# Kernel tuning notes

Measured on AMD Instinct MI355X. Metric: run time of the kernel, lower is better.

The kernel has to match this reference:

```python
import jax, jax.numpy as jnp
import numpy as np

N, E0 = 50000, 800000          # nodes, raw edges (self-loops appended in reference)
IN, H, C = 128, 8, 8           # in_channels, heads, out_channels per head
ED, T = 16, 96                 # edge_dim, temporal profile length
NEG_SLOPE = 0.2                # leaky relu slope
CW = 0.5                       # complementarity_weight


def setup_inputs() -> dict:
    key = jax.random.key(0)
    ks = jax.random.split(key, 12)
    def xavier(k, shape):
        fan_in, fan_out = shape[1], shape[0]
        lim = np.sqrt(6.0 / (fan_in + fan_out)).astype(np.float32)
        return jax.random.uniform(k, shape, jnp.float32, -lim, lim)
    return {
        "x": jax.random.normal(ks[0], (N, IN), jnp.float32),
        "edge_index": jax.random.randint(ks[1], (2, E0), 0, N, jnp.int64),
        "edge_attr": jax.random.normal(ks[2], (E0, ED), jnp.float32),
        "temporal_profiles": jax.random.normal(ks[3], (N, T), jnp.float32),
        "Wq": xavier(ks[4], (H * C, IN)),
        "Wk": xavier(ks[5], (H * C, IN)),
        "Wv": xavier(ks[6], (H * C, IN)),
        "We": xavier(ks[7], (H * C, ED)),
        "comp_W": xavier(ks[8], (H, 2 * IN)),
        "comp_b": jnp.zeros((H,), jnp.float32),
        "Wo": xavier(ks[9], (C, H * C)),
        "bo": jnp.zeros((C,), jnp.float32),
    }


def reference(x, edge_index, edge_attr, temporal_profiles,
              Wq, Wk, Wv, We, comp_W, comp_b, Wo, bo):
    n = x.shape[0]
    # ---- add self loops (PyG add_self_loops; edge_attr filled with 1.0) ----
    loops = jnp.arange(n, dtype=edge_index.dtype)
    ei = jnp.concatenate([edge_index, jnp.stack([loops, loops])], axis=1)
    ea = jnp.concatenate(
        [edge_attr, jnp.ones((n, edge_attr.shape[1]), edge_attr.dtype)], axis=0)
    src, dst = ei[0], ei[1]  # key/value side (j) = src, query side (i) = dst

    # ---- node projections [N, H, C] ----
    q = (x @ Wq.T).reshape(n, H, C)
    k = (x @ Wk.T).reshape(n, H, C)
    v = (x @ Wv.T).reshape(n, H, C)

    # ---- complementarity scores per edge ----
    tp = temporal_profiles
    tpn = (tp - tp.mean(axis=1, keepdims=True)) / \
          (tp.std(axis=1, ddof=1, keepdims=True) + 1e-8)  # torch std is unbiased
    correlation = (tpn[src] * tpn[dst]).mean(axis=1)       # [E]
    # Linear(2*IN -> H) on concat([x[src], x[dst]]) == split matmul per node
    a_node = x @ comp_W[:, :IN].T                          # [N, H]
    b_node = x @ comp_W[:, IN:].T                          # [N, H]
    learned = jnp.tanh(a_node[src] + b_node[dst] + comp_b).mean(axis=1)
    comp = 0.5 * correlation + 0.5 * learned               # [E]

    # ---- per-edge attention logits ----
    key_j = k[src]                                         # [E, H, C]
    alpha = (q[dst] * key_j).sum(-1) / np.sqrt(C).astype(np.float32)  # [E, H]
    edge_feat = (ea @ We.T).reshape(-1, H, C)
    alpha = alpha + (edge_feat * key_j).sum(-1)
    alpha = alpha + CW * (-comp)[:, None]
    alpha = jnp.where(alpha >= 0, alpha, NEG_SLOPE * alpha)  # leaky_relu

    # ---- segment softmax over destination nodes (PyG softmax) ----
    amax = jax.ops.segment_max(alpha, dst, num_segments=n)   # every node has a self loop
    e = jnp.exp(alpha - amax[dst])
    denom = jax.ops.segment_sum(e, dst, num_segments=n)
    att = e / (denom[dst] + 1e-16)                           # [E, H]

    # ---- weighted scatter-add aggregation ----
    msg = v[src] * att[:, :, None]                           # [E, H, C]
    out = jax.ops.segment_sum(msg, dst, num_segments=n).reshape(n, H * C)
    return out @ Wo.T + bo
```

## Files before the change

### kernel.cpp

```cpp
#include <hip/hip_runtime.h>
#include <math.h>


struct __align__(8) US4 { unsigned short x, y, z, w; };

typedef __attribute__((ext_vector_type(8))) short bf16x8;
typedef __attribute__((ext_vector_type(4))) float f32x4;

#define CH 32

__device__ __forceinline__ unsigned short f2bf(float f) {
    unsigned u = __float_as_uint(f);
    unsigned r = (u + 0x7fffu + ((u >> 16) & 1u)) >> 16;
    return (unsigned short)r;
}
__device__ __forceinline__ float bf2f(unsigned short u) {
    return __uint_as_float(((unsigned)u) << 16);
}
__device__ __forceinline__ float blo(unsigned u) { return __uint_as_float(u << 16); }
__device__ __forceinline__ float bhi(unsigned u) { return __uint_as_float(u & 0xffff0000u); }

__global__ __launch_bounds__(256) void k_xcvt(const float* __restrict__ x,
                                              unsigned short* __restrict__ xb, int total4)
{
    int i = blockIdx.x * 256 + threadIdx.x;
    if (i >= total4) return;
    float4 v = ((const float4*)x)[i];
    US4 u = { f2bf(v.x), f2bf(v.y), f2bf(v.z), f2bf(v.w) };
    ((US4*)xb)[i] = u;
}

__global__ __launch_bounds__(256) void k_bpack(
    const float* __restrict__ Wq, const float* __restrict__ Wk, const float* __restrict__ Wv,
    const float* __restrict__ compW, const float* __restrict__ We,
    unsigned short* __restrict__ Bp)
{
    int gid = blockIdx.x * 256 + threadIdx.x;
    if (gid >= 21 * 2048) return;
    int i = gid & 7, lane = (gid >> 3) & 63, s = (gid >> 9) & 3, t = gid >> 11;
    int col = t * 16 + (lane & 15);
    int k = s * 32 + ((lane >> 4) << 3) + i;
    float v;
    if (col < 64)        v = Wq[col * 128 + k];
    else if (col < 128)  v = Wk[(col - 64) * 128 + k];
    else if (col < 192)  v = Wv[(col - 128) * 128 + k];
    else if (col < 200)  v = compW[(col - 192) * 256 + k];
    else if (col < 208)  v = compW[(col - 200) * 256 + 128 + k];
    else {
        int hd = col - 208, h = hd >> 4, d = hd & 15;
        v = 0.f;
        #pragma unroll
        for (int c = 0; c < 8; c++)
            v += Wk[(h * 8 + c) * 128 + k] * We[(h * 8 + c) * 16 + d];
    }
    Bp[gid] = f2bf(v);
}

__global__ __launch_bounds__(256) void k_gemm(
    const unsigned short* __restrict__ xb, const unsigned short* __restrict__ Bp,
    const float* __restrict__ compb,
    float* __restrict__ q, unsigned short* __restrict__ kb, unsigned short* __restrict__ vb,
    float* __restrict__ an, float* __restrict__ bn, unsigned short* __restrict__ Gb, int N)
{
    const int tid = threadIdx.x, w = tid >> 6, lane = tid & 63;
    const int half = lane >> 4;
    const int c0 = lane & 15;
    int row_a = blockIdx.x * 64 + w * 16 + c0;
    int ra = min(row_a, N - 1);
    bf16x8 a0 = *(const bf16x8*)(xb + (size_t)ra * 128 +  0 + half * 8);
    bf16x8 a1 = *(const bf16x8*)(xb + (size_t)ra * 128 + 32 + half * 8);
    bf16x8 a2 = *(const bf16x8*)(xb + (size_t)ra * 128 + 64 + half * 8);
    bf16x8 a3 = *(const bf16x8*)(xb + (size_t)ra * 128 + 96 + half * 8);
    const int rbase = blockIdx.x * 64 + w * 16 + half * 4;
    const float cbv = compb[c0 & 7];

    for (int t = 0; t < 21; t++) {
        f32x4 acc = {0.f, 0.f, 0.f, 0.f};
        const bf16x8* bp = (const bf16x8*)(Bp + (size_t)((t * 4) * 64 + lane) * 8);
        acc = __builtin_amdgcn_mfma_f32_16x16x32_bf16(a0, bp[0],   acc, 0, 0, 0);
        acc = __builtin_amdgcn_mfma_f32_16x16x32_bf16(a1, bp[64],  acc, 0, 0, 0);
        acc = __builtin_amdgcn_mfma_f32_16x16x32_bf16(a2, bp[128], acc, 0, 0, 0);
        acc = __builtin_amdgcn_mfma_f32_16x16x32_bf16(a3, bp[192], acc, 0, 0, 0);
        #pragma unroll
        for (int r = 0; r < 4; r++) {
            int rr = rbase + r;
            if (rr >= N) continue;
            float vr = acc[r];
            if (t < 4)        q[(size_t)rr * 64 + t * 16 + c0] = vr * 0.35355339059327373f;
            else if (t < 8)   kb[(size_t)rr * 64 + (t - 4) * 16 + c0] = f2bf(vr);
            else if (t < 12)  vb[(size_t)rr * 64 + (t - 8) * 16 + c0] = f2bf(vr);
            else if (t == 12) {
                if (c0 < 8) an[(size_t)rr * 8 + c0] = vr;
                else        bn[(size_t)rr * 8 + (c0 - 8)] = vr + cbv;
            }
            else              Gb[(size_t)rr * 128 + (t - 13) * 16 + c0] = f2bf(vr);
        }
    }
}

__global__ __launch_bounds__(256) void k_tpn(const float* __restrict__ tp,
                                             unsigned short* __restrict__ tpnb, int N)
{
    int wave = threadIdx.x >> 6;
    int lane = threadIdx.x & 63;
    int n = blockIdx.x * 4 + wave;
    if (n >= N) return;
    const float* row = tp + (size_t)n * 96;
    float v0 = row[lane];
    float v1 = (lane < 32) ? row[64 + lane] : 0.f;
    float s = v0 + v1, ss = v0 * v0 + v1 * v1;
    #pragma unroll
    for (int m = 1; m < 64; m <<= 1) { s += __shfl_xor(s, m); ss += __shfl_xor(ss, m); }
    float mean = s * (1.f / 96.f);
    float var = (ss - 96.f * mean * mean) * (1.f / 95.f);
    var = fmaxf(var, 0.f);
    float inv = 1.f / (sqrtf(var) + 1e-8f);
    unsigned short* orow = tpnb + (size_t)n * 96;
    orow[lane] = f2bf((v0 - mean) * inv);
    if (lane < 32) orow[64 + lane] = f2bf((v1 - mean) * inv);
}

__global__ __launch_bounds__(256) void k_hist(const int* __restrict__ ei,
                                              int* __restrict__ deg,
                                              int* __restrict__ rnk, int E0, int N)
{
    int e = blockIdx.x * 256 + threadIdx.x;
    int E = E0 + N;
    if (e >= E) return;
    int dst = (e < E0) ? ei[E0 + e] : (e - E0);
    rnk[e] = atomicAdd(&deg[dst], 1);
}

__global__ __launch_bounds__(256) void k_scanA(const int* __restrict__ deg,
                                               int* __restrict__ bsum, int N)
{
    __shared__ int sm[256];
    int i = blockIdx.x * 256 + threadIdx.x;
    sm[threadIdx.x] = (i < N) ? deg[i] : 0;
    __syncthreads();
    for (int off = 128; off > 0; off >>= 1) {
        if (threadIdx.x < off) sm[threadIdx.x] += sm[threadIdx.x + off];
        __syncthreads();
    }
    if (threadIdx.x == 0) bsum[blockIdx.x] = sm[0];
}

__global__ __launch_bounds__(256) void k_scanB(int* __restrict__ bsum, int NB)
{
    __shared__ int sm[256];
    int t = threadIdx.x;
    sm[t] = (t < NB) ? bsum[t] : 0;
    __syncthreads();
    for (int off = 1; off < 256; off <<= 1) {
        int v = (t >= off) ? sm[t - off] : 0;
        __syncthreads();
        sm[t] += v;
        __syncthreads();
    }
    if (t < NB) bsum[t] = (t == 0) ? 0 : sm[t - 1];
}

__global__ __launch_bounds__(256) void k_scanC(const int* __restrict__ deg,
                                               const int* __restrict__ bsum,
                                               int* __restrict__ row, int N)
{
    __shared__ int sm[256];
    int b = blockIdx.x, t = threadIdx.x, i = b * 256 + t;
    int v = (i < N) ? deg[i] : 0;
    sm[t] = v;
    __syncthreads();
    for (int off = 1; off < 256; off <<= 1) {
        int u = (t >= off) ? sm[t - off] : 0;
        __syncthreads();
        sm[t] += u;
        __syncthreads();
    }
    int excl = bsum[b] + sm[t] - v;
    if (i < N) {
        row[i] = excl;
        if (i == N - 1) row[N] = excl + v;
    }
}

__global__ __launch_bounds__(256) void k_scatter(const int* __restrict__ ei,
                                                 const int* __restrict__ row,
                                                 const int* __restrict__ rnk,
                                                 int2* __restrict__ csrd, int E0, int N)
{
    int e = blockIdx.x * 256 + threadIdx.x;
    int E = E0 + N;
    if (e >= E) return;
    int src, dst;
    if (e < E0) { src = ei[e]; dst = ei[E0 + e]; }
    else        { src = e - E0; dst = src; }
    int pos = row[dst] + rnk[e];
    csrd[pos] = make_int2(e, src);
}

__global__ __launch_bounds__(256) void k_nodeattn(
    const int2* __restrict__ csrd, const int* __restrict__ row,
    const float* __restrict__ eattr,
    const unsigned short* __restrict__ tpnb, const float* __restrict__ q,
    const unsigned short* __restrict__ kb, const unsigned short* __restrict__ Gb,
    const float* __restrict__ an, const float* __restrict__ bn,
    const unsigned short* __restrict__ vb,
    const float* __restrict__ Wo, const float* __restrict__ bo,
    float* __restrict__ out, int E0, int N)
{
    __shared__ float alsA[4][CH * 8];
    __shared__ int srcA[4][CH];
    const int tid = threadIdx.x;
    const int wave = tid >> 6, lane = tid & 63;
    const int n = blockIdx.x * 4 + wave;
    if (n >= N) return;
    float* als = alsA[wave];
    int* srcs = srcA[wave];

    const int beg = row[n], end = row[n + 1];
    const int h = lane & 7;
    const int g = lane >> 3;

    const float4* qp = (const float4*)(q + (size_t)n * 64 + h * 8);
    const float4 qd0 = qp[0], qd1 = qp[1];
    const uint2* tdp = (const uint2*)(tpnb + (size_t)n * 96 + h * 12);
    const uint2 td0 = tdp[0], td1 = tdp[1], td2 = tdp[2];
    const float bnh = bn[(size_t)n * 8 + h];

    float m_reg = -1e30f, dsum = 0.f;
    float acc[8];
    #pragma unroll
    for (int c = 0; c < 8; c++) acc[c] = 0.f;

    for (int cbeg = beg; cbeg < end; cbeg += CH) {
        const int cnt = min(CH, end - cbeg);

        #pragma unroll
        for (int j = 0; j < 4; j++) {
            int eo = g + 8 * j;
            if (eo < cnt) {
                int2 es = csrd[cbeg + eo];
                const int e = es.x, s = es.y;

                const US4* kp = (const US4*)(kb + (size_t)s * 64 + h * 8);
                US4 k0 = kp[0], k1 = kp[1];
                float qk = qd0.x*bf2f(k0.x) + qd0.y*bf2f(k0.y) + qd0.z*bf2f(k0.z) + qd0.w*bf2f(k0.w)
                         + qd1.x*bf2f(k1.x) + qd1.y*bf2f(k1.y) + qd1.z*bf2f(k1.z) + qd1.w*bf2f(k1.w);

                const uint4* gp = (const uint4*)(Gb + (size_t)s * 128 + h * 16);
                uint4 g0 = gp[0], g1 = gp[1];
                int ec = (e < E0) ? e : 0;
                const float4* ep4 = (const float4*)(eattr + (size_t)ec * 16);
                float4 e0 = ep4[0], e1 = ep4[1], e2 = ep4[2], e3 = ep4[3];
                if (e >= E0) {
                    e0 = make_float4(1.f, 1.f, 1.f, 1.f); e1 = e0; e2 = e0; e3 = e0;
                }
                float efk = e0.x*blo(g0.x) + e0.y*bhi(g0.x) + e0.z*blo(g0.y) + e0.w*bhi(g0.y)
                          + e1.x*blo(g0.z) + e1.y*bhi(g0.z) + e1.z*blo(g0.w) + e1.w*bhi(g0.w)
                          + e2.x*blo(g1.x) + e2.y*bhi(g1.x) + e2.z*blo(g1.y) + e2.w*bhi(g1.y)
                          + e3.x*blo(g1.z) + e3.y*bhi(g1.z) + e3.z*blo(g1.w) + e3.w*bhi(g1.w);

                float tv = an[(size_t)s * 8 + h] + bnh;
                float ex = __expf(2.f * tv);
                float tn = 1.f - 2.f / (ex + 1.f);

                const uint2* tsp = (const uint2*)(tpnb + (size_t)s * 96 + h * 12);
                uint2 s0 = tsp[0], s1 = tsp[1], s2 = tsp[2];
                float pc = blo(s0.x)*blo(td0.x) + bhi(s0.x)*bhi(td0.x)
                         + blo(s0.y)*blo(td0.y) + bhi(s0.y)*bhi(td0.y)
                         + blo(s1.x)*blo(td1.x) + bhi(s1.x)*bhi(td1.x)
                         + blo(s1.y)*blo(td1.y) + bhi(s1.y)*bhi(td1.y)
                         + blo(s2.x)*blo(td2.x) + bhi(s2.x)*bhi(td2.x)
                         + blo(s2.y)*blo(td2.y) + bhi(s2.y)*bhi(td2.y);
                float cv = pc * (-0.25f / 96.f) + tn * (-0.25f / 8.f);
                cv += __shfl_xor(cv, 1); cv += __shfl_xor(cv, 2); cv += __shfl_xor(cv, 4);

                float a = qk + efk + cv;
                a = fmaxf(a, 0.2f * a);
                als[eo * 8 + h] = a;
                if (h == 0) srcs[eo] = s;
            }
        }

        float mloc = -1e30f;
        #pragma unroll
        for (int r = 0; r < 4; r++) {
            int eo = g + 8 * r;
            if (eo < cnt) mloc = fmaxf(mloc, als[eo * 8 + h]);
        }
        mloc = fmaxf(mloc, __shfl_xor(mloc, 8));
        mloc = fmaxf(mloc, __shfl_xor(mloc, 16));
        mloc = fmaxf(mloc, __shfl_xor(mloc, 32));

        float mn = fmaxf(m_reg, mloc);
        float sc = __expf(m_reg - mn);
        m_reg = mn;
        dsum *= sc;
        #pragma unroll
        for (int c = 0; c < 8; c++) acc[c] *= sc;

        for (int i = g; i < cnt; i += 8) {
            float av = als[i * 8 + h];
            int s = srcs[i];
            uint4 vu = *(const uint4*)(vb + (size_t)s * 64 + h * 8);
            float p = __expf(av - mn);
            dsum += p;
            acc[0] += p * blo(vu.x); acc[1] += p * bhi(vu.x);
            acc[2] += p * blo(vu.y); acc[3] += p * bhi(vu.y);
            acc[4] += p * blo(vu.z); acc[5] += p * bhi(vu.z);
            acc[6] += p * blo(vu.w); acc[7] += p * bhi(vu.w);
        }
    }

    dsum += __shfl_xor(dsum, 8); dsum += __shfl_xor(dsum, 16); dsum += __shfl_xor(dsum, 32);
    #pragma unroll
    for (int c = 0; c < 8; c++) {
        acc[c] += __shfl_xor(acc[c], 8);
        acc[c] += __shfl_xor(acc[c], 16);
        acc[c] += __shfl_xor(acc[c], 32);
    }
    float inv = 1.f / (dsum + 1e-16f);

    float po[8];
    #pragma unroll
    for (int cp8 = 0; cp8 < 8; cp8++) {
        const float4* wr = (const float4*)(Wo + cp8 * 64 + h * 8);
        float4 w0 = wr[0], w1 = wr[1];
        po[cp8] = inv * (acc[0]*w0.x + acc[1]*w0.y + acc[2]*w0.z + acc[3]*w0.w
                       + acc[4]*w1.x + acc[5]*w1.y + acc[6]*w1.z + acc[7]*w1.w);
    }
    #pragma unroll
    for (int cp8 = 0; cp8 < 8; cp8++) {
        po[cp8] += __shfl_xor(po[cp8], 1);
        po[cp8] += __shfl_xor(po[cp8], 2);
        po[cp8] += __shfl_xor(po[cp8], 4);
    }
    if (lane < 8) out[(size_t)n * 8 + lane] = po[lane] + bo[lane];
}

extern "C" void kernel_launch(void* const* d_in, const int* in_sizes, int n_in,
                              void* d_out, int out_size, void* d_ws, size_t ws_size,
                              hipStream_t stream)
{
    const float* x     = (const float*)d_in[0];
    const int*   ei    = (const int*)d_in[1];
    const float* eattr = (const float*)d_in[2];
    const float* tp    = (const float*)d_in[3];
    const float* Wq    = (const float*)d_in[4];
    const float* Wk    = (const float*)d_in[5];
    const float* Wv    = (const float*)d_in[6];
    const float* We    = (const float*)d_in[7];
    const float* compW = (const float*)d_in[8];
    const float* compb = (const float*)d_in[9];
    const float* Wo    = (const float*)d_in[10];
    const float* bo    = (const float*)d_in[11];
    float* out = (float*)d_out;

    const int N  = in_sizes[0] / 128;
    const int E0 = in_sizes[1] / 2;
    const int E  = E0 + N;
    const int NB = (N + 255) / 256;

    float* ws = (float*)d_ws;
    size_t off = 0;
    unsigned short* tpnb = (unsigned short*)(ws + off); off += (size_t)N * 48;
    float* q  = ws + off; off += (size_t)N * 64;
    unsigned short* kb = (unsigned short*)(ws + off); off += (size_t)N * 32;
    unsigned short* vb = (unsigned short*)(ws + off); off += (size_t)N * 32;
    unsigned short* Gb = (unsigned short*)(ws + off); off += (size_t)N * 64;
    float* an = ws + off; off += (size_t)N * 8;
    float* bn = ws + off; off += (size_t)N * 8;
    int* deg    = (int*)(ws + off); off += N;
    int* bsum   = (int*)(ws + off); off += 256;
    int* rowp   = (int*)(ws + off); off += N + 4;
    unsigned short* Bp = (unsigned short*)(ws + off); off += 21504;
    int2* csrd  = (int2*)(ws + off); off += (size_t)E * 2;
    int* rnk    = (int*)(ws + off); off += E;
    unsigned short* xb = (unsigned short*)(ws + off); off += (size_t)N * 64;

    hipMemsetAsync(deg, 0, (size_t)N * sizeof(int), stream);

    k_hist<<<(E + 255) / 256, 256, 0, stream>>>(ei, deg, rnk, E0, N);
    k_scanA<<<NB, 256, 0, stream>>>(deg, bsum, N);
    k_scanB<<<1, 256, 0, stream>>>(bsum, NB);
    k_scanC<<<NB, 256, 0, stream>>>(deg, bsum, rowp, N);
    k_scatter<<<(E + 255) / 256, 256, 0, stream>>>(ei, rowp, rnk, csrd, E0, N);

    k_xcvt<<<((size_t)N * 32 + 255) / 256, 256, 0, stream>>>(x, xb, N * 32);
    k_bpack<<<(21 * 2048 + 255) / 256, 256, 0, stream>>>(Wq, Wk, Wv, compW, We, Bp);
    k_gemm<<<(N + 63) / 64, 256, 0, stream>>>(xb, Bp, compb, q, kb, vb, an, bn, Gb, N);
    k_tpn<<<(N + 3) / 4, 256, 0, stream>>>(tp, tpnb, N);

    k_nodeattn<<<(N + 3) / 4, 256, 0, stream>>>(csrd, rowp, eattr, tpnb, q, kb, Gb,
                                                an, bn, vb, Wo, bo, out, E0, N);
}
```

Measured before the change: 228.8 us.

## Fuse x bf16 conversion into GEMM and keep attention logits in registers

```diff
diff --git a/kernel.cpp b/kernel.cpp
--- a/kernel.cpp
+++ b/kernel.cpp
@@ -19,16 +19,6 @@
 }
 __device__ __forceinline__ float blo(unsigned u) { return __uint_as_float(u << 16); }
 __device__ __forceinline__ float bhi(unsigned u) { return __uint_as_float(u & 0xffff0000u); }
-
-__global__ __launch_bounds__(256) void k_xcvt(const float* __restrict__ x,
-                                              unsigned short* __restrict__ xb, int total4)
-{
-    int i = blockIdx.x * 256 + threadIdx.x;
-    if (i >= total4) return;
-    float4 v = ((const float4*)x)[i];
-    US4 u = { f2bf(v.x), f2bf(v.y), f2bf(v.z), f2bf(v.w) };
-    ((US4*)xb)[i] = u;
-}
 
 __global__ __launch_bounds__(256) void k_bpack(
     const float* __restrict__ Wq, const float* __restrict__ Wk, const float* __restrict__ Wv,
@@ -56,8 +46,18 @@
     Bp[gid] = f2bf(v);
 }
 
+__device__ __forceinline__ bf16x8 ld_bf8(const float* p) {
+    float4 a = ((const float4*)p)[0], b = ((const float4*)p)[1];
+    bf16x8 r;
+    r[0] = (short)f2bf(a.x); r[1] = (short)f2bf(a.y);
+    r[2] = (short)f2bf(a.z); r[3] = (short)f2bf(a.w);
+    r[4] = (short)f2bf(b.x); r[5] = (short)f2bf(b.y);
+    r[6] = (short)f2bf(b.z); r[7] = (short)f2bf(b.w);
+    return r;
+}
+
 __global__ __launch_bounds__(256) void k_gemm(
-    const unsigned short* __restrict__ xb, const unsigned short* __restrict__ Bp,
+    const float* __restrict__ x, const unsigned short* __restrict__ Bp,
     const float* __restrict__ compb,
     float* __restrict__ q, unsigned short* __restrict__ kb, unsigned short* __restrict__ vb,
     float* __restrict__ an, float* __restrict__ bn, unsigned short* __restrict__ Gb, int N)
@@ -67,10 +67,11 @@
     const int c0 = lane & 15;
     int row_a = blockIdx.x * 64 + w * 16 + c0;
     int ra = min(row_a, N - 1);
-    bf16x8 a0 = *(const bf16x8*)(xb + (size_t)ra * 128 +  0 + half * 8);
-    bf16x8 a1 = *(const bf16x8*)(xb + (size_t)ra * 128 + 32 + half * 8);
-    bf16x8 a2 = *(const bf16x8*)(xb + (size_t)ra * 128 + 64 + half * 8);
-    bf16x8 a3 = *(const bf16x8*)(xb + (size_t)ra * 128 + 96 + half * 8);
+    const float* xr = x + (size_t)ra * 128 + half * 8;
+    bf16x8 a0 = ld_bf8(xr +  0);
+    bf16x8 a1 = ld_bf8(xr + 32);
+    bf16x8 a2 = ld_bf8(xr + 64);
+    bf16x8 a3 = ld_bf8(xr + 96);
     const int rbase = blockIdx.x * 64 + w * 16 + half * 4;
     const float cbv = compb[c0 & 7];
 
@@ -207,14 +208,10 @@
     const float* __restrict__ Wo, const float* __restrict__ bo,
     float* __restrict__ out, int E0, int N)
 {
-    __shared__ float alsA[4][CH * 8];
-    __shared__ int srcA[4][CH];
     const int tid = threadIdx.x;
     const int wave = tid >> 6, lane = tid & 63;
     const int n = blockIdx.x * 4 + wave;
     if (n >= N) return;
-    float* als = alsA[wave];
-    int* srcs = srcA[wave];
 
     const int beg = row[n], end = row[n + 1];
     const int h = lane & 7;
@@ -234,12 +231,18 @@
     for (int cbeg = beg; cbeg < end; cbeg += CH) {
         const int cnt = min(CH, end - cbeg);
 
+        float av[4];
+        uint4 vu[4];
         #pragma unroll
         for (int j = 0; j < 4; j++) {
+            av[j] = -1e30f;
+            vu[j] = make_uint4(0u, 0u, 0u, 0u);
             int eo = g + 8 * j;
             if (eo < cnt) {
                 int2 es = csrd[cbeg + eo];
                 const int e = es.x, s = es.y;
+
+                vu[j] = *(const uint4*)(vb + (size_t)s * 64 + h * 8);
 
                 const US4* kp = (const US4*)(kb + (size_t)s * 64 + h * 8);
                 US4 k0 = kp[0], k1 = kp[1];
@@ -275,18 +278,11 @@
                 cv += __shfl_xor(cv, 1); cv += __shfl_xor(cv, 2); cv += __shfl_xor(cv, 4);
 
                 float a = qk + efk + cv;
-                a = fmaxf(a, 0.2f * a);
-                als[eo * 8 + h] = a;
-                if (h == 0) srcs[eo] = s;
+                av[j] = fmaxf(a, 0.2f * a);
             }
         }
 
-        float mloc = -1e30f;
-        #pragma unroll
-        for (int r = 0; r < 4; r++) {
-            int eo = g + 8 * r;
-            if (eo < cnt) mloc = fmaxf(mloc, als[eo * 8 + h]);
-        }
+        float mloc = fmaxf(fmaxf(av[0], av[1]), fmaxf(av[2], av[3]));
         mloc = fmaxf(mloc, __shfl_xor(mloc, 8));
         mloc = fmaxf(mloc, __shfl_xor(mloc, 16));
         mloc = fmaxf(mloc, __shfl_xor(mloc, 32));
@@ -298,16 +294,14 @@
         #pragma unroll
         for (int c = 0; c < 8; c++) acc[c] *= sc;
 
-        for (int i = g; i < cnt; i += 8) {
-            float av = als[i * 8 + h];
-            int s = srcs[i];
-            uint4 vu = *(const uint4*)(vb + (size_t)s * 64 + h * 8);
-            float p = __expf(av - mn);
+        #pragma unroll
+        for (int j = 0; j < 4; j++) {
+            float p = __expf(av[j] - mn);
             dsum += p;
-            acc[0] += p * blo(vu.x); acc[1] += p * bhi(vu.x);
-            acc[2] += p * blo(vu.y); acc[3] += p * bhi(vu.y);
-            acc[4] += p * blo(vu.z); acc[5] += p * bhi(vu.z);
-            acc[6] += p * blo(vu.w); acc[7] += p * bhi(vu.w);
+            acc[0] += p * blo(vu[j].x); acc[1] += p * bhi(vu[j].x);
+            acc[2] += p * blo(vu[j].y); acc[3] += p * bhi(vu[j].y);
+            acc[4] += p * blo(vu[j].z); acc[5] += p * bhi(vu[j].z);
+            acc[6] += p * blo(vu[j].w); acc[7] += p * bhi(vu[j].w);
         }
     }
 
@@ -375,7 +369,6 @@
     unsigned short* Bp = (unsigned short*)(ws + off); off += 21504;
     int2* csrd  = (int2*)(ws + off); off += (size_t)E * 2;
     int* rnk    = (int*)(ws + off); off += E;
-    unsigned short* xb = (unsigned short*)(ws + off); off += (size_t)N * 64;
 
     hipMemsetAsync(deg, 0, (size_t)N * sizeof(int), stream);
 
@@ -385,9 +378,8 @@
     k_scanC<<<NB, 256, 0, stream>>>(deg, bsum, rowp, N);
     k_scatter<<<(E + 255) / 256, 256, 0, stream>>>(ei, rowp, rnk, csrd, E0, N);
 
-    k_xcvt<<<((size_t)N * 32 + 255) / 256, 256, 0, stream>>>(x, xb, N * 32);
     k_bpack<<<(21 * 2048 + 255) / 256, 256, 0, stream>>>(Wq, Wk, Wv, compW, We, Bp);
-    k_gemm<<<(N + 63) / 64, 256, 0, stream>>>(xb, Bp, compb, q, kb, vb, an, bn, Gb, N);
+    k_gemm<<<(N + 63) / 64, 256, 0, stream>>>(x, Bp, compb, q, kb, vb, an, bn, Gb, N);
     k_tpn<<<(N + 3) / 4, 256, 0, stream>>>(tp, tpnb, N);
 
     k_nodeattn<<<(N + 3) / 4, 256, 0, stream>>>(csrd, rowp, eattr, tpnb, q, kb, Gb,
```

After: 221.9 us. -3.0%, faster.
